# Kernel optimization log

Measured on AMD Instinct MI355X. Metric: run time of the kernel, lower is better.

The kernel has to match this reference:

```python
import jax, jax.numpy as jnp
import numpy as np


def _qkernel(r, i, j, k):
    # Build the real-valued block kernel of a quaternion dense layer.
    # r,i,j,k: [in/4, out/4] -> kernel [in, out] implementing the Hamilton product.
    col_r = jnp.concatenate([r, -i, -j, -k], axis=0)
    col_i = jnp.concatenate([i, r, -k, j], axis=0)
    col_j = jnp.concatenate([j, k, r, -i], axis=0)
    col_k = jnp.concatenate([k, -j, i, r], axis=0)
    return jnp.concatenate([col_r, col_i, col_j, col_k], axis=1)


def setup_inputs() -> dict:
    key = jax.random.key(0)
    ks = jax.random.split(key, 12)
    B, F, H = 32768, 1024, 256
    F4, H4 = F // 4, H // 4
    s_in = 1.0 / np.sqrt(F)
    s_h = 1.0 / np.sqrt(H)
    inp = {
        "x": jax.random.normal(ks[0], (B, F), dtype=jnp.float32),
        "wx_r": jax.random.normal(ks[1], (4, F4, H4), dtype=jnp.float32) * s_in,
        "wx_i": jax.random.normal(ks[2], (4, F4, H4), dtype=jnp.float32) * s_in,
        "wx_j": jax.random.normal(ks[3], (4, F4, H4), dtype=jnp.float32) * s_in,
        "wx_k": jax.random.normal(ks[4], (4, F4, H4), dtype=jnp.float32) * s_in,
        "bx": jnp.zeros((4, H), dtype=jnp.float32),
        "uh_r": jax.random.normal(ks[5], (4, H4, H4), dtype=jnp.float32) * s_h,
        "uh_i": jax.random.normal(ks[6], (4, H4, H4), dtype=jnp.float32) * s_h,
        "uh_j": jax.random.normal(ks[7], (4, H4, H4), dtype=jnp.float32) * s_h,
        "uh_k": jax.random.normal(ks[8], (4, H4, H4), dtype=jnp.float32) * s_h,
        "fco_w": jax.random.normal(ks[9], (H, H), dtype=jnp.float32) * s_h,
        "fco_b": jnp.zeros((H,), dtype=jnp.float32),
    }
    return inp


def reference(x, wx_r, wx_i, wx_j, wx_k, bx, uh_r, uh_i, uh_j, uh_k, fco_w, fco_b):
    # Single-step quaternion LSTM cell with zero initial hidden/cell state.
    # Gate order along leading axis: [forget, input, output, cell].
    Kx = jax.vmap(_qkernel)(wx_r, wx_i, wx_j, wx_k)   # [4, F, H]
    Ku = jax.vmap(_qkernel)(uh_r, uh_i, uh_j, uh_k)   # [4, H, H]
    H = bx.shape[1]
    h0 = jnp.zeros((x.shape[0], H), dtype=x.dtype)
    c0 = h0
    gx = jnp.einsum('bf,gfh->gbh', x, Kx) + bx[:, None, :]   # [4, B, H]
    gu = jnp.einsum('bh,ghk->gbk', h0, Ku)                    # [4, B, H]
    z = gx + gu
    ft = jax.nn.sigmoid(z[0])
    it = jax.nn.sigmoid(z[1])
    ot = jax.nn.sigmoid(z[2])
    at = z[3]
    c = it * jnp.tanh(at) + ft * c0
    h = ot * jnp.tanh(c)
    return h @ fco_w + fco_b
```

## Files before the change

kernel.cpp:

```cpp
#include <hip/hip_runtime.h>
#include <cstdint>
#include <cstddef>

#define WS_WP   0
#define WS_FCO  1572864
#define WS_BP   1703936
#define WS_HVP  1707008

typedef __attribute__((ext_vector_type(8))) __bf16 bf16x8;
typedef __attribute__((ext_vector_type(4))) float floatx4;

__device__ __forceinline__ unsigned short f2bf(float f) {
  unsigned int u = __builtin_bit_cast(unsigned int, f);
  u += 0x7fffu + ((u >> 16) & 1u);
  return (unsigned short)(u >> 16);
}

__device__ __forceinline__ float sigmf(float z) {
  return __builtin_amdgcn_rcpf(1.f + __expf(-z));
}
__device__ __forceinline__ float tanh_(float z) {
  return 1.f - 2.f * __builtin_amdgcn_rcpf(1.f + __expf(2.f * z));
}

__device__ __forceinline__ void gld16(const void* g, void* l) {
  __builtin_amdgcn_global_load_lds(
      (const __attribute__((address_space(1))) unsigned int*)g,
      (__attribute__((address_space(3))) unsigned int*)l, 16, 0, 0);
}

__global__ __launch_bounds__(256) void pack_w_k(
    const float* __restrict__ wr, const float* __restrict__ wi,
    const float* __restrict__ wj, const float* __restrict__ wk,
    const float* __restrict__ bx, unsigned short* __restrict__ Wp,
    float* __restrict__ bp) {
  int id = blockIdx.x * 256 + threadIdx.x;
  int c = id >> 7, oct = id & 127;
  int gp = c % 3 + 1;
  int h = c / 3;
  int hb = h >> 6, hr = h & 63;
  int f0 = oct << 3;
  int fb = f0 >> 8, fr0 = f0 & 255;
  const int   comp_t[4][4] = {{0,1,2,3},{1,0,3,2},{2,3,0,1},{3,2,1,0}};
  const float sign_t[4][4] = {{1.f,-1.f,-1.f,-1.f},{1.f,1.f,-1.f,1.f},
                              {1.f,1.f,1.f,-1.f},{1.f,-1.f,1.f,1.f}};
  const float* srcs[4] = {wr, wi, wj, wk};
  const float* s = srcs[comp_t[hb][fb]] + ((size_t)((gp << 8) + fr0)) * 64 + hr;
  float sg = sign_t[hb][fb];
  unsigned short v[8];
#pragma unroll
  for (int j = 0; j < 8; ++j) v[j] = f2bf(sg * s[(size_t)j * 64]);
  int cb = c / 192, nl = c % 192;
  int kb = f0 >> 5, q = (f0 >> 3) & 3;
  int idx16 = (nl << 2) + (q ^ ((nl >> 1) & 3));
  unsigned short* dst = Wp + (size_t)(cb * 32 + kb) * 6144 + idx16 * 8;
  uint4 val = make_uint4(
      (unsigned)v[0] | ((unsigned)v[1] << 16), (unsigned)v[2] | ((unsigned)v[3] << 16),
      (unsigned)v[4] | ((unsigned)v[5] << 16), (unsigned)v[6] | ((unsigned)v[7] << 16));
  *(uint4*)dst = val;
  if (oct == 0) bp[c] = bx[(gp << 8) + h];
}

__global__ __launch_bounds__(256) void pack_fco_k(
    const float* __restrict__ fw, unsigned short* __restrict__ Fp) {
  int id = blockIdx.x * 256 + threadIdx.x;
  int n = id >> 5, oct = id & 31;
  int k0 = oct << 3;
  unsigned short v[8];
#pragma unroll
  for (int j = 0; j < 8; ++j) v[j] = f2bf(fw[(size_t)(k0 + j) * 256 + n]);
  int nb = n >> 7, nl = n & 127, kb = oct >> 2, q = oct & 3;
  int idx16 = (nl << 2) + (q ^ ((nl >> 1) & 3));
  unsigned short* dst = Fp + (size_t)((nb << 3) + kb) * 4096 + idx16 * 8;
  uint4 val = make_uint4(
      (unsigned)v[0] | ((unsigned)v[1] << 16), (unsigned)v[2] | ((unsigned)v[3] << 16),
      (unsigned)v[4] | ((unsigned)v[5] << 16), (unsigned)v[6] | ((unsigned)v[7] << 16));
  *(uint4*)dst = val;
}

__global__ __launch_bounds__(256, 2) void gemm1_k(
    const float* __restrict__ x, const unsigned short* __restrict__ Wp,
    const float* __restrict__ bp, unsigned short* __restrict__ hvp) {
  __shared__ char smem[51456];
  float* sAf = (float*)smem;
  unsigned short* sBs = (unsigned short*)(smem + 16384);
  float* zep = (float*)smem;

  const int t = threadIdx.x;
  const int lane = t & 63, wid = t >> 6;
  const int wm = wid >> 1, wn = wid & 1;
  const int lrow = lane & 15, q = lane >> 4;
  const int row0 = blockIdx.x * 128;
  const int cby = blockIdx.y;
  const float* xbase = x + (size_t)row0 * 1024;

  floatx4 acc[4][6];
#pragma unroll
  for (int i = 0; i < 4; ++i)
#pragma unroll
    for (int j = 0; j < 6; ++j) acc[i][j] = (floatx4){0.f, 0.f, 0.f, 0.f};

  for (int kt = 0; kt < 32; ++kt) {
    const int k0 = kt * 32;
#pragma unroll
    for (int i = 0; i < 4; ++i) {
      int s = t + i * 256;
      int m = s >> 3, j = s & 7, jj = j ^ (m & 7);
      gld16(xbase + (size_t)m * 1024 + k0 + jj * 4, sAf + s * 4);
    }
    const unsigned short* bt = Wp + (size_t)(cby * 32 + kt) * 6144;
#pragma unroll
    for (int i = 0; i < 3; ++i) {
      int s = t + i * 256;
      gld16(bt + s * 8, sBs + s * 8);
    }
    __syncthreads();
    bf16x8 af[4], bf[6];
#pragma unroll
    for (int mt = 0; mt < 4; ++mt) {
      int m = wm * 64 + mt * 16 + lrow;
      const float4 a0 = *(const float4*)(sAf + (m * 8 + ((2 * q) ^ (m & 7))) * 4);
      const float4 a1 = *(const float4*)(sAf + (m * 8 + ((2 * q + 1) ^ (m & 7))) * 4);
      bf16x8 v;
      v[0] = (__bf16)a0.x; v[1] = (__bf16)a0.y; v[2] = (__bf16)a0.z; v[3] = (__bf16)a0.w;
      v[4] = (__bf16)a1.x; v[5] = (__bf16)a1.y; v[6] = (__bf16)a1.z; v[7] = (__bf16)a1.w;
      af[mt] = v;
    }
#pragma unroll
    for (int nt = 0; nt < 6; ++nt) {
      int n = wn * 96 + nt * 16 + lrow;
      int off16 = (n << 2) + (q ^ ((n >> 1) & 3));
      bf[nt] = *(const bf16x8*)(const void*)(sBs + off16 * 8);
    }
#pragma unroll
    for (int mt = 0; mt < 4; ++mt)
#pragma unroll
      for (int nt = 0; nt < 6; ++nt)
        acc[mt][nt] = __builtin_amdgcn_mfma_f32_16x16x32_bf16(af[mt], bf[nt], acc[mt][nt], 0, 0, 0);
    __syncthreads();
  }

  const float* bp0 = bp + cby * 192;
  const int er = t >> 2, oc = t & 3;
#pragma unroll
  for (int pass = 0; pass < 2; ++pass) {
    if (wm == pass) {
#pragma unroll
      for (int mt = 0; mt < 4; ++mt)
#pragma unroll
        for (int nt = 0; nt < 6; ++nt)
#pragma unroll
          for (int r = 0; r < 4; ++r)
            zep[(mt * 16 + q * 4 + r) * 201 + wn * 96 + nt * 16 + lrow] = acc[mt][nt][r];
    }
    __syncthreads();
    int ml = pass * 64 + er;
#pragma unroll
    for (int half = 0; half < 2; ++half) {
      int oo = oc + half * 4;
      unsigned short v[8];
#pragma unroll
      for (int j = 0; j < 8; ++j) {
        int hl = oo * 8 + j;
        float zi = zep[er * 201 + hl * 3 + 0] + bp0[hl * 3 + 0];
        float zo = zep[er * 201 + hl * 3 + 1] + bp0[hl * 3 + 1];
        float zc = zep[er * 201 + hl * 3 + 2] + bp0[hl * 3 + 2];
        float it = sigmf(zi);
        float ot = sigmf(zo);
        float cc = it * tanh_(zc);
        v[j] = f2bf(ot * tanh_(cc));
      }
      int ktile = cby * 2 + (oo >> 2), qq = oo & 3;
      int idx16 = (ml << 2) + (qq ^ ((ml >> 1) & 3));
      uint4 val = make_uint4(
          (unsigned)v[0] | ((unsigned)v[1] << 16), (unsigned)v[2] | ((unsigned)v[3] << 16),
          (unsigned)v[4] | ((unsigned)v[5] << 16), (unsigned)v[6] | ((unsigned)v[7] << 16));
      *(uint4*)(hvp + (size_t)(blockIdx.x * 8 + ktile) * 4096 + idx16 * 8) = val;
    }
    __syncthreads();
  }
}

__global__ __launch_bounds__(256, 3) void gemm2_k(
    const unsigned short* __restrict__ hvp, const unsigned short* __restrict__ Fp,
    const float* __restrict__ fcob, float* __restrict__ out) {
  __shared__ char smem[16384];
  unsigned short* sA = (unsigned short*)smem;
  unsigned short* sB = (unsigned short*)(smem + 8192);
  const int t = threadIdx.x;
  const int lane = t & 63, wid = t >> 6;
  const int wm = wid >> 1, wn = wid & 1;
  const int lrow = lane & 15, q = lane >> 4;
  const int mb = blockIdx.x, nb = blockIdx.y;

  floatx4 acc[4][4];
#pragma unroll
  for (int i = 0; i < 4; ++i)
#pragma unroll
    for (int j = 0; j < 4; ++j) acc[i][j] = (floatx4){0.f, 0.f, 0.f, 0.f};

  for (int kt = 0; kt < 8; ++kt) {
    const unsigned short* at_ = hvp + (size_t)(mb * 8 + kt) * 4096;
    const unsigned short* bt_ = Fp + (size_t)(nb * 8 + kt) * 4096;
    gld16(at_ + t * 8, sA + t * 8);
    gld16(at_ + 2048 + t * 8, sA + 2048 + t * 8);
    gld16(bt_ + t * 8, sB + t * 8);
    gld16(bt_ + 2048 + t * 8, sB + 2048 + t * 8);
    __syncthreads();
    bf16x8 af[4], bf[4];
#pragma unroll
    for (int mt = 0; mt < 4; ++mt) {
      int m = wm * 64 + mt * 16 + lrow;
      int o = (m << 2) + (q ^ ((m >> 1) & 3));
      af[mt] = *(const bf16x8*)(const void*)(sA + o * 8);
    }
#pragma unroll
    for (int nt = 0; nt < 4; ++nt) {
      int n = wn * 64 + nt * 16 + lrow;
      int o = (n << 2) + (q ^ ((n >> 1) & 3));
      bf[nt] = *(const bf16x8*)(const void*)(sB + o * 8);
    }
#pragma unroll
    for (int mt = 0; mt < 4; ++mt)
#pragma unroll
      for (int nt = 0; nt < 4; ++nt)
        acc[mt][nt] = __builtin_amdgcn_mfma_f32_16x16x32_bf16(af[mt], bf[nt], acc[mt][nt], 0, 0, 0);
    __syncthreads();
  }
#pragma unroll
  for (int nt = 0; nt < 4; ++nt) {
    int colg = nb * 128 + wn * 64 + nt * 16 + lrow;
    float bias = fcob[colg];
#pragma unroll
    for (int mt = 0; mt < 4; ++mt) {
      int rowg = mb * 128 + wm * 64 + mt * 16 + q * 4;
#pragma unroll
      for (int r = 0; r < 4; ++r)
        out[(size_t)(rowg + r) * 256 + colg] = acc[mt][nt][r] + bias;
    }
  }
}

extern "C" void kernel_launch(void* const* d_in, const int* in_sizes, int n_in,
                              void* d_out, int out_size, void* d_ws, size_t ws_size,
                              hipStream_t stream) {
  const float* x  = (const float*)d_in[0];
  const float* wr = (const float*)d_in[1];
  const float* wi = (const float*)d_in[2];
  const float* wj = (const float*)d_in[3];
  const float* wk = (const float*)d_in[4];
  const float* bx = (const float*)d_in[5];
  const float* fw = (const float*)d_in[10];
  const float* fb = (const float*)d_in[11];
  char* ws = (char*)d_ws;
  unsigned short* Wp  = (unsigned short*)(ws + WS_WP);
  unsigned short* Fp  = (unsigned short*)(ws + WS_FCO);
  float*          bp  = (float*)(ws + WS_BP);
  unsigned short* hvp = (unsigned short*)(ws + WS_HVP);
  float*          out = (float*)d_out;

  hipLaunchKernelGGL(pack_w_k,   dim3(384),    dim3(256), 0, stream, wr, wi, wj, wk, bx, Wp, bp);
  hipLaunchKernelGGL(pack_fco_k, dim3(32),     dim3(256), 0, stream, fw, Fp);
  hipLaunchKernelGGL(gemm1_k,    dim3(256, 4), dim3(256), 0, stream, x, Wp, bp, hvp);
  hipLaunchKernelGGL(gemm2_k,    dim3(256, 2), dim3(256), 0, stream, hvp, Fp, fb, out);
}
```

Baseline: 295.8 us.

## Halve gemm1 N-tile for occupancy, merge pack kernels, keep fco weights in LDS

Gemm1 now computes 96 gate columns per block instead of 192, with a grid of 8 column blocks. This shrinks the accumulators and LDS so four blocks can share a CU, at the cost of rereading the x tile twice as often. The two weight-packing kernels are merged into one launch with a coalesced thread mapping. Gemm2 loads its whole 128-column slice of fco weights into LDS once and reads the A operand straight from global memory, which removes the per-k-step barriers.

```diff
diff --git a/kernel.cpp b/kernel.cpp
--- a/kernel.cpp
+++ b/kernel.cpp
@@ -29,59 +29,59 @@
       (__attribute__((address_space(3))) unsigned int*)l, 16, 0, 0);
 }
 
-__global__ __launch_bounds__(256) void pack_w_k(
+__global__ __launch_bounds__(256) void pack_k(
     const float* __restrict__ wr, const float* __restrict__ wi,
     const float* __restrict__ wj, const float* __restrict__ wk,
-    const float* __restrict__ bx, unsigned short* __restrict__ Wp,
+    const float* __restrict__ bx, const float* __restrict__ fw,
+    unsigned short* __restrict__ Wp, unsigned short* __restrict__ Fp,
     float* __restrict__ bp) {
-  int id = blockIdx.x * 256 + threadIdx.x;
-  int c = id >> 7, oct = id & 127;
-  int gp = c % 3 + 1;
-  int h = c / 3;
-  int hb = h >> 6, hr = h & 63;
-  int f0 = oct << 3;
-  int fb = f0 >> 8, fr0 = f0 & 255;
-  const int   comp_t[4][4] = {{0,1,2,3},{1,0,3,2},{2,3,0,1},{3,2,1,0}};
-  const float sign_t[4][4] = {{1.f,-1.f,-1.f,-1.f},{1.f,1.f,-1.f,1.f},
-                              {1.f,1.f,1.f,-1.f},{1.f,-1.f,1.f,1.f}};
-  const float* srcs[4] = {wr, wi, wj, wk};
-  const float* s = srcs[comp_t[hb][fb]] + ((size_t)((gp << 8) + fr0)) * 64 + hr;
-  float sg = sign_t[hb][fb];
-  unsigned short v[8];
-#pragma unroll
-  for (int j = 0; j < 8; ++j) v[j] = f2bf(sg * s[(size_t)j * 64]);
-  int cb = c / 192, nl = c % 192;
-  int kb = f0 >> 5, q = (f0 >> 3) & 3;
-  int idx16 = (nl << 2) + (q ^ ((nl >> 1) & 3));
-  unsigned short* dst = Wp + (size_t)(cb * 32 + kb) * 6144 + idx16 * 8;
-  uint4 val = make_uint4(
-      (unsigned)v[0] | ((unsigned)v[1] << 16), (unsigned)v[2] | ((unsigned)v[3] << 16),
-      (unsigned)v[4] | ((unsigned)v[5] << 16), (unsigned)v[6] | ((unsigned)v[7] << 16));
-  *(uint4*)dst = val;
-  if (oct == 0) bp[c] = bx[(gp << 8) + h];
-}
-
-__global__ __launch_bounds__(256) void pack_fco_k(
-    const float* __restrict__ fw, unsigned short* __restrict__ Fp) {
-  int id = blockIdx.x * 256 + threadIdx.x;
-  int n = id >> 5, oct = id & 31;
-  int k0 = oct << 3;
-  unsigned short v[8];
-#pragma unroll
-  for (int j = 0; j < 8; ++j) v[j] = f2bf(fw[(size_t)(k0 + j) * 256 + n]);
-  int nb = n >> 7, nl = n & 127, kb = oct >> 2, q = oct & 3;
-  int idx16 = (nl << 2) + (q ^ ((nl >> 1) & 3));
-  unsigned short* dst = Fp + (size_t)((nb << 3) + kb) * 4096 + idx16 * 8;
-  uint4 val = make_uint4(
-      (unsigned)v[0] | ((unsigned)v[1] << 16), (unsigned)v[2] | ((unsigned)v[3] << 16),
-      (unsigned)v[4] | ((unsigned)v[5] << 16), (unsigned)v[6] | ((unsigned)v[7] << 16));
-  *(uint4*)dst = val;
-}
-
-__global__ __launch_bounds__(256, 2) void gemm1_k(
+  int t = threadIdx.x;
+  if (blockIdx.x < 384) {
+    int gpp = blockIdx.x >> 7;
+    int oct = blockIdx.x & 127;
+    int gp = gpp + 1;
+    int h = t;
+    int hb = h >> 6, hr = h & 63;
+    int f0 = oct << 3;
+    int fb = f0 >> 8, fr0 = f0 & 255;
+    const int   comp_t[4][4] = {{0,1,2,3},{1,0,3,2},{2,3,0,1},{3,2,1,0}};
+    const float sign_t[4][4] = {{1.f,-1.f,-1.f,-1.f},{1.f,1.f,-1.f,1.f},
+                                {1.f,1.f,1.f,-1.f},{1.f,-1.f,1.f,1.f}};
+    const float* srcs[4] = {wr, wi, wj, wk};
+    const float* s = srcs[comp_t[hb][fb]] + ((size_t)((gp << 8) + fr0)) * 64 + hr;
+    float sg = sign_t[hb][fb];
+    unsigned short v[8];
+#pragma unroll
+    for (int j = 0; j < 8; ++j) v[j] = f2bf(sg * s[(size_t)j * 64]);
+    int c = h * 3 + gpp;
+    int cb = c / 96, nl = c % 96;
+    int kb = oct >> 2, q = oct & 3;
+    int idx16 = (nl << 2) + (q ^ ((nl >> 1) & 3));
+    uint4 val = make_uint4(
+        (unsigned)v[0] | ((unsigned)v[1] << 16), (unsigned)v[2] | ((unsigned)v[3] << 16),
+        (unsigned)v[4] | ((unsigned)v[5] << 16), (unsigned)v[6] | ((unsigned)v[7] << 16));
+    *(uint4*)(Wp + (size_t)(cb * 32 + kb) * 3072 + idx16 * 8) = val;
+    if (oct == 0) bp[c] = bx[(gp << 8) + h];
+  } else {
+    int oct = blockIdx.x - 384;
+    int n = t;
+    int k0 = oct << 3;
+    unsigned short v[8];
+#pragma unroll
+    for (int j = 0; j < 8; ++j) v[j] = f2bf(fw[(size_t)(k0 + j) * 256 + n]);
+    int nb = n >> 7, nl = n & 127, kb = oct >> 2, q = oct & 3;
+    int idx16 = (nl << 2) + (q ^ ((nl >> 1) & 3));
+    uint4 val = make_uint4(
+        (unsigned)v[0] | ((unsigned)v[1] << 16), (unsigned)v[2] | ((unsigned)v[3] << 16),
+        (unsigned)v[4] | ((unsigned)v[5] << 16), (unsigned)v[6] | ((unsigned)v[7] << 16));
+    *(uint4*)(Fp + (size_t)((nb << 3) + kb) * 4096 + idx16 * 8) = val;
+  }
+}
+
+__global__ __launch_bounds__(256, 4) void gemm1_k(
     const float* __restrict__ x, const unsigned short* __restrict__ Wp,
     const float* __restrict__ bp, unsigned short* __restrict__ hvp) {
-  __shared__ char smem[51456];
+  __shared__ char smem[22528];
   float* sAf = (float*)smem;
   unsigned short* sBs = (unsigned short*)(smem + 16384);
   float* zep = (float*)smem;
@@ -94,11 +94,11 @@
   const int cby = blockIdx.y;
   const float* xbase = x + (size_t)row0 * 1024;
 
-  floatx4 acc[4][6];
+  floatx4 acc[4][3];
 #pragma unroll
   for (int i = 0; i < 4; ++i)
 #pragma unroll
-    for (int j = 0; j < 6; ++j) acc[i][j] = (floatx4){0.f, 0.f, 0.f, 0.f};
+    for (int j = 0; j < 3; ++j) acc[i][j] = (floatx4){0.f, 0.f, 0.f, 0.f};
 
   for (int kt = 0; kt < 32; ++kt) {
     const int k0 = kt * 32;
@@ -108,14 +108,11 @@
       int m = s >> 3, j = s & 7, jj = j ^ (m & 7);
       gld16(xbase + (size_t)m * 1024 + k0 + jj * 4, sAf + s * 4);
     }
-    const unsigned short* bt = Wp + (size_t)(cby * 32 + kt) * 6144;
-#pragma unroll
-    for (int i = 0; i < 3; ++i) {
-      int s = t + i * 256;
-      gld16(bt + s * 8, sBs + s * 8);
-    }
-    __syncthreads();
-    bf16x8 af[4], bf[6];
+    const unsigned short* bt = Wp + (size_t)(cby * 32 + kt) * 3072;
+    gld16(bt + t * 8, sBs + t * 8);
+    if (t < 128) gld16(bt + 2048 + t * 8, sBs + 2048 + t * 8);
+    __syncthreads();
+    bf16x8 af[4], bf[3];
 #pragma unroll
     for (int mt = 0; mt < 4; ++mt) {
       int m = wm * 64 + mt * 16 + lrow;
@@ -127,105 +124,100 @@
       af[mt] = v;
     }
 #pragma unroll
-    for (int nt = 0; nt < 6; ++nt) {
-      int n = wn * 96 + nt * 16 + lrow;
+    for (int nt = 0; nt < 3; ++nt) {
+      int n = wn * 48 + nt * 16 + lrow;
       int off16 = (n << 2) + (q ^ ((n >> 1) & 3));
       bf[nt] = *(const bf16x8*)(const void*)(sBs + off16 * 8);
     }
 #pragma unroll
     for (int mt = 0; mt < 4; ++mt)
 #pragma unroll
-      for (int nt = 0; nt < 6; ++nt)
+      for (int nt = 0; nt < 3; ++nt)
         acc[mt][nt] = __builtin_amdgcn_mfma_f32_16x16x32_bf16(af[mt], bf[nt], acc[mt][nt], 0, 0, 0);
     __syncthreads();
   }
 
-  const float* bp0 = bp + cby * 192;
-  const int er = t >> 2, oc = t & 3;
-#pragma unroll
-  for (int pass = 0; pass < 2; ++pass) {
-    if (wm == pass) {
-#pragma unroll
-      for (int mt = 0; mt < 4; ++mt)
-#pragma unroll
-        for (int nt = 0; nt < 6; ++nt)
+  const float* bp0 = bp + cby * 96;
+  const int row_ip = t >> 3, ho = t & 7;
+  unsigned short* hvt = hvp + (size_t)(blockIdx.x * 8 + cby) * 4096;
+#pragma unroll
+  for (int p = 0; p < 4; ++p) {
+    if (wm == (p >> 1)) {
+#pragma unroll
+      for (int mt2 = 0; mt2 < 2; ++mt2) {
+        int mt = (p & 1) * 2 + mt2;
+#pragma unroll
+        for (int nt = 0; nt < 3; ++nt)
 #pragma unroll
           for (int r = 0; r < 4; ++r)
-            zep[(mt * 16 + q * 4 + r) * 201 + wn * 96 + nt * 16 + lrow] = acc[mt][nt][r];
-    }
-    __syncthreads();
-    int ml = pass * 64 + er;
-#pragma unroll
-    for (int half = 0; half < 2; ++half) {
-      int oo = oc + half * 4;
-      unsigned short v[8];
-#pragma unroll
-      for (int j = 0; j < 8; ++j) {
-        int hl = oo * 8 + j;
-        float zi = zep[er * 201 + hl * 3 + 0] + bp0[hl * 3 + 0];
-        float zo = zep[er * 201 + hl * 3 + 1] + bp0[hl * 3 + 1];
-        float zc = zep[er * 201 + hl * 3 + 2] + bp0[hl * 3 + 2];
-        float it = sigmf(zi);
-        float ot = sigmf(zo);
-        float cc = it * tanh_(zc);
-        v[j] = f2bf(ot * tanh_(cc));
+            zep[(mt2 * 16 + q * 4 + r) * 100 + wn * 48 + nt * 16 + lrow] = acc[mt][nt][r];
       }
-      int ktile = cby * 2 + (oo >> 2), qq = oo & 3;
-      int idx16 = (ml << 2) + (qq ^ ((ml >> 1) & 3));
-      uint4 val = make_uint4(
-          (unsigned)v[0] | ((unsigned)v[1] << 16), (unsigned)v[2] | ((unsigned)v[3] << 16),
-          (unsigned)v[4] | ((unsigned)v[5] << 16), (unsigned)v[6] | ((unsigned)v[7] << 16));
-      *(uint4*)(hvp + (size_t)(blockIdx.x * 8 + ktile) * 4096 + idx16 * 8) = val;
-    }
-    __syncthreads();
-  }
-}
-
-__global__ __launch_bounds__(256, 3) void gemm2_k(
+    }
+    __syncthreads();
+    unsigned short v[4];
+#pragma unroll
+    for (int j = 0; j < 4; ++j) {
+      int hl = ho * 4 + j;
+      float zi = zep[row_ip * 100 + hl * 3 + 0] + bp0[hl * 3 + 0];
+      float zo = zep[row_ip * 100 + hl * 3 + 1] + bp0[hl * 3 + 1];
+      float zc = zep[row_ip * 100 + hl * 3 + 2] + bp0[hl * 3 + 2];
+      float it = sigmf(zi);
+      float ot = sigmf(zo);
+      float cc = it * tanh_(zc);
+      v[j] = f2bf(ot * tanh_(cc));
+    }
+    int ml = p * 32 + row_ip;
+    int qq = ho >> 1;
+    int idx16 = (ml << 2) + (qq ^ ((ml >> 1) & 3));
+    uint2 val = make_uint2((unsigned)v[0] | ((unsigned)v[1] << 16),
+                           (unsigned)v[2] | ((unsigned)v[3] << 16));
+    *(uint2*)(hvt + (size_t)idx16 * 8 + (ho & 1) * 4) = val;
+    __syncthreads();
+  }
+}
+
+__global__ __launch_bounds__(256, 4) void gemm2_k(
     const unsigned short* __restrict__ hvp, const unsigned short* __restrict__ Fp,
     const float* __restrict__ fcob, float* __restrict__ out) {
-  __shared__ char smem[16384];
-  unsigned short* sA = (unsigned short*)smem;
-  unsigned short* sB = (unsigned short*)(smem + 8192);
+  __shared__ unsigned short sB[32768];
   const int t = threadIdx.x;
   const int lane = t & 63, wid = t >> 6;
   const int wm = wid >> 1, wn = wid & 1;
   const int lrow = lane & 15, q = lane >> 4;
   const int mb = blockIdx.x, nb = blockIdx.y;
 
+  const unsigned short* fpb = Fp + (size_t)nb * 32768;
+#pragma unroll
+  for (int i = 0; i < 16; ++i) gld16(fpb + (t + i * 256) * 8, sB + (t + i * 256) * 8);
+
   floatx4 acc[4][4];
 #pragma unroll
   for (int i = 0; i < 4; ++i)
 #pragma unroll
     for (int j = 0; j < 4; ++j) acc[i][j] = (floatx4){0.f, 0.f, 0.f, 0.f};
-
+  __syncthreads();
+
+#pragma unroll
   for (int kt = 0; kt < 8; ++kt) {
     const unsigned short* at_ = hvp + (size_t)(mb * 8 + kt) * 4096;
-    const unsigned short* bt_ = Fp + (size_t)(nb * 8 + kt) * 4096;
-    gld16(at_ + t * 8, sA + t * 8);
-    gld16(at_ + 2048 + t * 8, sA + 2048 + t * 8);
-    gld16(bt_ + t * 8, sB + t * 8);
-    gld16(bt_ + 2048 + t * 8, sB + 2048 + t * 8);
-    __syncthreads();
     bf16x8 af[4], bf[4];
 #pragma unroll
     for (int mt = 0; mt < 4; ++mt) {
       int m = wm * 64 + mt * 16 + lrow;
       int o = (m << 2) + (q ^ ((m >> 1) & 3));
-      af[mt] = *(const bf16x8*)(const void*)(sA + o * 8);
+      af[mt] = *(const bf16x8*)(const void*)(at_ + o * 8);
     }
 #pragma unroll
     for (int nt = 0; nt < 4; ++nt) {
       int n = wn * 64 + nt * 16 + lrow;
       int o = (n << 2) + (q ^ ((n >> 1) & 3));
-      bf[nt] = *(const bf16x8*)(const void*)(sB + o * 8);
+      bf[nt] = *(const bf16x8*)(const void*)(sB + kt * 4096 + o * 8);
     }
 #pragma unroll
     for (int mt = 0; mt < 4; ++mt)
 #pragma unroll
       for (int nt = 0; nt < 4; ++nt)
         acc[mt][nt] = __builtin_amdgcn_mfma_f32_16x16x32_bf16(af[mt], bf[nt], acc[mt][nt], 0, 0, 0);
-    __syncthreads();
   }
 #pragma unroll
   for (int nt = 0; nt < 4; ++nt) {
@@ -259,8 +251,7 @@
   unsigned short* hvp = (unsigned short*)(ws + WS_HVP);
   float*          out = (float*)d_out;
 
-  hipLaunchKernelGGL(pack_w_k,   dim3(384),    dim3(256), 0, stream, wr, wi, wj, wk, bx, Wp, bp);
-  hipLaunchKernelGGL(pack_fco_k, dim3(32),     dim3(256), 0, stream, fw, Fp);
-  hipLaunchKernelGGL(gemm1_k,    dim3(256, 4), dim3(256), 0, stream, x, Wp, bp, hvp);
-  hipLaunchKernelGGL(gemm2_k,    dim3(256, 2), dim3(256), 0, stream, hvp, Fp, fb, out);
-}
+  hipLaunchKernelGGL(pack_k,  dim3(416),    dim3(256), 0, stream, wr, wi, wj, wk, bx, fw, Wp, Fp, bp);
+  hipLaunchKernelGGL(gemm1_k, dim3(256, 8), dim3(256), 0, stream, x, Wp, bp, hvp);
+  hipLaunchKernelGGL(gemm2_k, dim3(256, 2), dim3(256), 0, stream, hvp, Fp, fb, out);
+}
```

Result: slower. 308.7 us (+4.4%).
